# Performance work log

Measured on AMD Instinct MI355X. Metric: run time of the kernel, lower is better.

The kernel has to match this reference:

```python
import jax, jax.numpy as jnp
import numpy as np

EMBED = 1024
HEADS = 16
B, T = 2, 1024


def setup_inputs() -> dict:
    key = jax.random.key(0)
    k1, k2 = jax.random.split(key)
    x = jax.random.normal(k1, (B, T, EMBED), dtype=jnp.float32)
    # causal mask: True positions are masked to -inf (torch masked_fill semantics)
    mask = jnp.triu(jnp.ones((T, T), dtype=bool), k=1)
    weight = jax.random.normal(k2, (HEADS * EMBED, EMBED), dtype=jnp.float32)
    return {"x": x, "mask": mask, "weight": weight}


def reference(x, mask, weight):
    b, t, c = x.shape
    h = weight.shape[0] // c  # num_heads
    # split channels into heads: (b, h, t, head_dim)
    y = x.reshape(b, t, h, c // h).transpose(0, 2, 1, 3)
    # per-head scores (b, h, t, t)
    s = jnp.einsum('bhtk,bhsk->bhts', y, y)
    # mask BEFORE scaling, then scale by sqrt(num_heads) (not head_dim!)
    s = jnp.where(mask, -jnp.inf, s)
    p = jax.nn.softmax(s / jnp.sqrt(jnp.asarray(h, dtype=s.dtype)), axis=-1)
    # V is raw x broadcast across heads: (b, h, t, c)
    o = jnp.einsum('bhts,bsc->bhtc', p, x)
    # concat heads -> (b, t, h*c), final linear
    o = o.transpose(0, 2, 1, 3).reshape(b, t, h * c)
    return o @ weight
```

## Files before the change

### kernel.cpp

```cpp
#include <hip/hip_runtime.h>
#include <hip/hip_bf16.h>

#define B_ 2
#define T_ 1024
#define C_ 1024
#define H_ 16

typedef short bf16x8 __attribute__((ext_vector_type(8)));
typedef float f32x4 __attribute__((ext_vector_type(4)));

#define MFMA16(a, b, c) __builtin_amdgcn_mfma_f32_16x16x32_bf16(a, b, c, 0, 0, 0)

__device__ inline short f2bf(float x) {
    union { __hip_bfloat16 h; short s; } u;
    u.h = __float2bfloat16(x);
    return u.s;
}

__device__ inline void gl_lds16(const void* g, void* l) {
    __builtin_amdgcn_global_load_lds(
        (const __attribute__((address_space(1))) unsigned int*)g,
        (__attribute__((address_space(3))) unsigned int*)l, 16, 0, 0);
}

__global__ __launch_bounds__(256) void cvt_x(const float* __restrict__ x,
                                             short* __restrict__ xb) {
    int idx = (blockIdx.x * 256 + threadIdx.x) * 8;
    float4 a = *(const float4*)(x + idx);
    float4 b = *(const float4*)(x + idx + 4);
    bf16x8 v;
    v[0] = f2bf(a.x); v[1] = f2bf(a.y); v[2] = f2bf(a.z); v[3] = f2bf(a.w);
    v[4] = f2bf(b.x); v[5] = f2bf(b.y); v[6] = f2bf(b.z); v[7] = f2bf(b.w);
    *(bf16x8*)(xb + idx) = v;
}

__global__ __launch_bounds__(256) void cvt_w(const float* __restrict__ W,
                                             short* __restrict__ Wt) {
    __shared__ float T[64][65];
    const int bid = blockIdx.x;
    const int nb = bid & 15, cb = (bid >> 4) & 15, h = bid >> 8;
    const int t = threadIdx.x;
    const int c0 = cb * 64, n0 = nb * 64;
    const float* src = W + (size_t)(h * 1024 + c0) * 1024 + n0;
    {
        const int cl = t >> 4, nl = (t & 15) * 4;
#pragma unroll
        for (int r = 0; r < 4; ++r) {
            float4 v = *(const float4*)(src + (size_t)(cl + r * 16) * 1024 + nl);
            T[cl + r * 16][nl + 0] = v.x;
            T[cl + r * 16][nl + 1] = v.y;
            T[cl + r * 16][nl + 2] = v.z;
            T[cl + r * 16][nl + 3] = v.w;
        }
    }
    __syncthreads();
    {
        short* dst = Wt + (size_t)(h * 1024 + n0) * 1024 + c0;
        const int nl = t >> 3, cl8 = (t & 7) * 8;
#pragma unroll
        for (int r = 0; r < 2; ++r) {
            const int n = nl + r * 32;
            bf16x8 o;
#pragma unroll
            for (int j = 0; j < 8; ++j) o[j] = f2bf(T[cl8 + j][n]);
            *(bf16x8*)(dst + (size_t)n * 1024 + cl8) = o;
        }
    }
}

__global__ __launch_bounds__(512, 2) void attn_po(const short* __restrict__ xb,
                                                  const short* __restrict__ xbT,
                                                  short* __restrict__ O) {
    __shared__ short Pb[2][64][72];
    __shared__ float row_al[2][64];
    __shared__ float row_l[64];
    __shared__ int   flags[2][4];

    const int tid = threadIdx.x;
    const int bh = blockIdx.x & 31;
    const int rest = blockIdx.x >> 5;
    const int tb = (rest < 8) ? rest : 23 - rest;
    const int b = bh >> 4, h = bh & 15;
    const int lane = tid & 63, q = lane >> 4, l16 = lane & 15;
    const int w = tid >> 6;
    const int g = w & 3;
    const int nw = w * 128;
    const short* xbb = xb + ((size_t)b << 20);
    const short* vtb = xbT + ((size_t)b << 20);

    const int t0 = tb * 64;
    const int nch = tb + 1;

    f32x4 acc[4][8];
#pragma unroll
    for (int mt = 0; mt < 4; ++mt)
#pragma unroll
        for (int nt = 0; nt < 8; ++nt) acc[mt][nt] = (f32x4){0.f, 0.f, 0.f, 0.f};
    float m_r[4], l_r[4];
#pragma unroll
    for (int r = 0; r < 4; ++r) { m_r[r] = -3.0e38f; l_r[r] = 0.f; }

    bf16x8 qf[2];
    if (w < 4) {
#pragma unroll
        for (int ks = 0; ks < 2; ++ks)
            qf[ks] = *(const bf16x8*)(xbb + (size_t)(t0 + g * 16 + l16) * 1024 +
                                      h * 64 + ks * 32 + q * 8);
    }

    for (int ci = -1; ci < nch; ++ci) {
        __syncthreads();
        const int cc = ci + 1;
        if (w < 4 && cc < nch) {
            const int s0 = (cc == 0) ? t0 : (cc - 1) * 64;
            const int par = cc & 1;
            f32x4 sf[4];
#pragma unroll
            for (int st = 0; st < 4; ++st) sf[st] = (f32x4){0.f, 0.f, 0.f, 0.f};
#pragma unroll
            for (int st = 0; st < 4; ++st)
#pragma unroll
                for (int ks = 0; ks < 2; ++ks) {
                    bf16x8 kf = *(const bf16x8*)(xbb +
                        (size_t)(s0 + st * 16 + l16) * 1024 + h * 64 + ks * 32 + q * 8);
                    sf[st] = MFMA16(qf[ks], kf, sf[st]);
                }
            float mx[4] = {-3.0e38f, -3.0e38f, -3.0e38f, -3.0e38f};
#pragma unroll
            for (int st = 0; st < 4; ++st)
#pragma unroll
                for (int r = 0; r < 4; ++r) {
                    float v = sf[st][r] * 0.25f;
                    if (cc == 0 && (s0 + st * 16 + l16) > (t0 + g * 16 + q * 4 + r))
                        v = -3.0e38f;
                    sf[st][r] = v;
                    mx[r] = fmaxf(mx[r], v);
                }
#pragma unroll
            for (int r = 0; r < 4; ++r) {
                mx[r] = fmaxf(mx[r], __shfl_xor(mx[r], 1));
                mx[r] = fmaxf(mx[r], __shfl_xor(mx[r], 2));
                mx[r] = fmaxf(mx[r], __shfl_xor(mx[r], 4));
                mx[r] = fmaxf(mx[r], __shfl_xor(mx[r], 8));
            }
            float sum[4], al[4];
            int upd = 0;
#pragma unroll
            for (int r = 0; r < 4; ++r) {
                float m_new = fmaxf(m_r[r], mx[r]);
                al[r] = __expf(m_r[r] - m_new);
                upd |= (m_new > m_r[r]) ? 1 : 0;
                m_r[r] = m_new;
                sum[r] = 0.f;
            }
#pragma unroll
            for (int st = 0; st < 4; ++st)
#pragma unroll
                for (int r = 0; r < 4; ++r) {
                    float pv = __expf(sf[st][r] - m_r[r]);
                    sum[r] += pv;
                    Pb[par][g * 16 + q * 4 + r][st * 16 + l16] = f2bf(pv);
                }
#pragma unroll
            for (int r = 0; r < 4; ++r) {
                sum[r] += __shfl_xor(sum[r], 1);
                sum[r] += __shfl_xor(sum[r], 2);
                sum[r] += __shfl_xor(sum[r], 4);
                sum[r] += __shfl_xor(sum[r], 8);
                l_r[r] = l_r[r] * al[r] + sum[r];
            }
            if (l16 == 0) {
#pragma unroll
                for (int r = 0; r < 4; ++r) row_al[par][g * 16 + q * 4 + r] = al[r];
            }
            int any_upd = __any(upd);
            if (lane == 0) flags[par][g] = any_upd;
        }
        if (ci >= 0) {
            const int par = ci & 1;
            if (flags[par][0] | flags[par][1] | flags[par][2] | flags[par][3]) {
#pragma unroll
                for (int mt = 0; mt < 4; ++mt) {
                    float a0 = row_al[par][mt * 16 + q * 4 + 0];
                    float a1 = row_al[par][mt * 16 + q * 4 + 1];
                    float a2 = row_al[par][mt * 16 + q * 4 + 2];
                    float a3 = row_al[par][mt * 16 + q * 4 + 3];
#pragma unroll
                    for (int nt = 0; nt < 8; ++nt) {
                        acc[mt][nt][0] *= a0;
                        acc[mt][nt][1] *= a1;
                        acc[mt][nt][2] *= a2;
                        acc[mt][nt][3] *= a3;
                    }
                }
            }
            bf16x8 pf[4][2];
#pragma unroll
            for (int mt = 0; mt < 4; ++mt)
#pragma unroll
                for (int ks = 0; ks < 2; ++ks)
                    pf[mt][ks] = *(bf16x8*)&Pb[par][mt * 16 + l16][ks * 32 + q * 8];
            const int s0p = (ci == 0) ? t0 : (ci - 1) * 64;
#pragma unroll
            for (int nt = 0; nt < 8; ++nt)
#pragma unroll
                for (int ks = 0; ks < 2; ++ks) {
                    bf16x8 vf = *(const bf16x8*)(vtb +
                        (size_t)(nw + nt * 16 + l16) * 1024 + s0p + ks * 32 + q * 8);
#pragma unroll
                    for (int mt = 0; mt < 4; ++mt)
                        acc[mt][nt] = MFMA16(pf[mt][ks], vf, acc[mt][nt]);
                }
        }
    }

    if (w < 4 && l16 == 0) {
#pragma unroll
        for (int r = 0; r < 4; ++r) row_l[g * 16 + q * 4 + r] = l_r[r];
    }
    __syncthreads();
    short* ob = O + ((((size_t)(b * 1024 + t0) * 16) + h) << 10);
#pragma unroll
    for (int mt = 0; mt < 4; ++mt) {
        float i0 = 1.f / row_l[mt * 16 + q * 4 + 0];
        float i1 = 1.f / row_l[mt * 16 + q * 4 + 1];
        float i2 = 1.f / row_l[mt * 16 + q * 4 + 2];
        float i3 = 1.f / row_l[mt * 16 + q * 4 + 3];
#pragma unroll
        for (int nt = 0; nt < 8; ++nt) {
            size_t base = (size_t)(mt * 16 + q * 4) * 16384 + nw + nt * 16 + l16;
            ob[base]         = f2bf(acc[mt][nt][0] * i0);
            ob[base + 16384] = f2bf(acc[mt][nt][1] * i1);
            ob[base + 32768] = f2bf(acc[mt][nt][2] * i2);
            ob[base + 49152] = f2bf(acc[mt][nt][3] * i3);
        }
    }
}

__global__ __launch_bounds__(256, 4) void ogemm(const short* __restrict__ O,
                                                const short* __restrict__ Wt,
                                                float* __restrict__ out) {
    __shared__ short Al[8][128][8];
    __shared__ short Bl[8][128][8];

    const int orig = blockIdx.x;
    const int x = orig & 7, j = orig >> 3;
    const int kq  = x >> 1;
    const int m_t = (x & 1) * 8 + (j >> 3);
    const int n_t = j & 7;
    const int m0 = m_t * 128, n0 = n_t * 128;
    const int t = threadIdx.x;
    const int lane = t & 63, q = lane >> 4, l16 = lane & 15;
    const int wv = t >> 6;
    const int wm = (wv & 1) * 64, wn = (wv >> 1) * 64;

    const short* Ab = O + (size_t)m0 * 16384;
    const int srow = t & 127, skg = t >> 7;

    char* al_base = (char*)&Al[0][0][0] + (size_t)t * 16;
    char* bl_base = (char*)&Bl[0][0][0] + (size_t)t * 16;

    f32x4 acc[4][4];
#pragma unroll
    for (int i = 0; i < 4; ++i)
#pragma unroll
        for (int j2 = 0; j2 < 4; ++j2) acc[i][j2] = (f32x4){0.f, 0.f, 0.f, 0.f};

    const int kbase = kq * 4096;
    for (int kk = 0; kk < 4096; kk += 64) {
        const int k0 = kbase + kk;
        const int h = k0 >> 10, c0 = k0 & 1023;
        const short* Arow = Ab + (size_t)srow * 16384 + k0;
        const short* Brow = Wt + ((size_t)h << 20) + (size_t)(n0 + srow) * 1024 + c0;
        __syncthreads();
#pragma unroll
        for (int jj = 0; jj < 4; ++jj) {
            gl_lds16(Arow + (2 * jj + skg) * 8, al_base + jj * 4096);
            gl_lds16(Brow + (2 * jj + skg) * 8, bl_base + jj * 4096);
        }
        __syncthreads();
#pragma unroll
        for (int ks = 0; ks < 2; ++ks) {
            bf16x8 af[4], bfr[4];
#pragma unroll
            for (int i = 0; i < 4; ++i)
                af[i] = *(bf16x8*)&Al[q + 4 * ks][wm + i * 16 + l16][0];
#pragma unroll
            for (int j2 = 0; j2 < 4; ++j2)
                bfr[j2] = *(bf16x8*)&Bl[q + 4 * ks][wn + j2 * 16 + l16][0];
#pragma unroll
            for (int i = 0; i < 4; ++i)
#pragma unroll
                for (int j2 = 0; j2 < 4; ++j2)
                    acc[i][j2] = MFMA16(af[i], bfr[j2], acc[i][j2]);
        }
    }

#pragma unroll
    for (int i = 0; i < 4; ++i)
#pragma unroll
        for (int j2 = 0; j2 < 4; ++j2)
#pragma unroll
            for (int r = 0; r < 4; ++r) {
                int m = m0 + wm + i * 16 + q * 4 + r;
                int n = n0 + wn + j2 * 16 + l16;
                atomicAdd(out + (size_t)m * 1024 + n, acc[i][j2][r]);
            }
}

__global__ __launch_bounds__(256, 4) void zgemm_fast(const short* __restrict__ xb,
                                                     const short* __restrict__ Wt,
                                                     short* __restrict__ ZT) {
    __shared__ short Al[4][128][8];
    __shared__ short Bl[4][128][8];

    const int bid = blockIdx.x;
    const int n_t = bid & 7, h = (bid >> 3) & 15, s_t = bid >> 7;
    const int n0 = n_t * 128, s0g = s_t * 128;
    const int t = threadIdx.x;
    const int lane = t & 63, q = lane >> 4, l16 = lane & 15;
    const int wv = t >> 6;
    const int wm = (wv & 1) * 64, wn = (wv >> 1) * 64;

    const short* Ab = Wt + ((size_t)h * 1024 + n0) * 1024;
    const short* Bb = xb + (size_t)s0g * 1024;
    const int srow = t & 127, skg = t >> 7;

    char* al_base = (char*)&Al[0][0][0] + (size_t)t * 16;
    char* bl_base = (char*)&Bl[0][0][0] + (size_t)t * 16;

    f32x4 acc[4][4];
#pragma unroll
    for (int i = 0; i < 4; ++i)
#pragma unroll
        for (int j = 0; j < 4; ++j) acc[i][j] = (f32x4){0.f, 0.f, 0.f, 0.f};

    for (int k0 = 0; k0 < 1024; k0 += 32) {
        __syncthreads();
        gl_lds16(Ab + (size_t)srow * 1024 + k0 + skg * 8, al_base);
        gl_lds16(Ab + (size_t)srow * 1024 + k0 + (skg + 2) * 8, al_base + 4096);
        gl_lds16(Bb + (size_t)srow * 1024 + k0 + skg * 8, bl_base);
        gl_lds16(Bb + (size_t)srow * 1024 + k0 + (skg + 2) * 8, bl_base + 4096);
        __syncthreads();
        bf16x8 af[4], bfr[4];
#pragma unroll
        for (int i = 0; i < 4; ++i) af[i] = *(bf16x8*)&Al[q][wm + i * 16 + l16][0];
#pragma unroll
        for (int j = 0; j < 4; ++j) bfr[j] = *(bf16x8*)&Bl[q][wn + j * 16 + l16][0];
#pragma unroll
        for (int i = 0; i < 4; ++i)
#pragma unroll
            for (int j = 0; j < 4; ++j)
                acc[i][j] = MFMA16(af[i], bfr[j], acc[i][j]);
    }

    const int b = s0g >> 10, s_in0 = s0g & 1023;
    short* zb = ZT + ((size_t)(b * 16 + h) << 20);
#pragma unroll
    for (int i = 0; i < 4; ++i)
#pragma unroll
        for (int j = 0; j < 4; ++j)
#pragma unroll
            for (int r = 0; r < 4; ++r) {
                int n = n0 + wm + i * 16 + q * 4 + r;
                int s = s_in0 + wn + j * 16 + l16;
                zb[(size_t)n * 1024 + s] = f2bf(acc[i][j][r]);
            }
}

#define ZPAD 40

__global__ __launch_bounds__(256, 2) void zgemm_sm(const short* __restrict__ xb,
                                                   const float* __restrict__ W,
                                                   short* __restrict__ ZT) {
    __shared__ short Wts[128 * ZPAD];
    __shared__ short Xs[2][128 * ZPAD];

    const int tid = threadIdx.x;
    const int bs = blockIdx.x & 7;
    const int bn = (blockIdx.x >> 3) & 7;
    const int h  = blockIdx.x >> 6;
    const int s0 = bs * 128, n0 = bn * 128;
    const int lane = tid & 63, q = lane >> 4, l16 = lane & 15;
    const int w = tid >> 6, bw = w >> 1, sh = w & 1;

    f32x4 acc[8][4];
#pragma unroll
    for (int i = 0; i < 8; ++i)
#pragma unroll
        for (int j = 0; j < 4; ++j) acc[i][j] = (f32x4){0.f, 0.f, 0.f, 0.f};

    for (int k0 = 0; k0 < 1024; k0 += 32) {
        __syncthreads();
#pragma unroll
        for (int r = 0; r < 2; ++r) {
            const int c2 = ((tid >> 5) << 1) + (r << 4);
            const float* w0p = W + (size_t)(h * 1024 + k0 + c2) * 1024 + n0;
            const float* w1p = w0p + 1024;
#pragma unroll
            for (int i = 0; i < 4; ++i) {
                const int n = (tid & 31) + (i << 5);
                float wa = w0p[n], wb = w1p[n];
                unsigned u = (unsigned)(unsigned short)f2bf(wa) |
                             ((unsigned)(unsigned short)f2bf(wb) << 16);
                *(unsigned*)&Wts[n * ZPAD + c2] = u;
            }
        }
#pragma unroll
        for (int i = 0; i < 4; ++i) {
            const int id = tid + (i << 8);
            const int b2 = id >> 9, s = (id >> 2) & 127, cg = id & 3;
            bf16x8 v = *(const bf16x8*)(xb + (size_t)b2 * (T_ * C_) +
                                        (size_t)(s0 + s) * 1024 + k0 + cg * 8);
            *(bf16x8*)&Xs[b2][s * ZPAD + cg * 8] = v;
        }
        __syncthreads();

        bf16x8 af[8], bfr[4];
#pragma unroll
        for (int nt = 0; nt < 8; ++nt)
            af[nt] = *(bf16x8*)&Wts[(nt * 16 + l16) * ZPAD + q * 8];
#pragma unroll
        for (int st = 0; st < 4; ++st)
            bfr[st] = *(bf16x8*)&Xs[bw][(sh * 64 + st * 16 + l16) * ZPAD + q * 8];
#pragma unroll
        for (int nt = 0; nt < 8; ++nt)
#pragma unroll
            for (int st = 0; st < 4; ++st)
                acc[nt][st] = MFMA16(af[nt], bfr[st], acc[nt][st]);
    }

    short* zb = ZT + (size_t)(bw * 16 + h) * (1024 * 1024);
#pragma unroll
    for (int nt = 0; nt < 8; ++nt)
#pragma unroll
        for (int st = 0; st < 4; ++st)
#pragma unroll
            for (int r = 0; r < 4; ++r) {
                int n_abs = n0 + nt * 16 + q * 4 + r;
                int s_abs = s0 + sh * 64 + st * 16 + l16;
                zb[(size_t)n_abs * 1024 + s_abs] = f2bf(acc[nt][st][r]);
            }
}

__global__ __launch_bounds__(512, 2) void attn(const short* __restrict__ xb,
                                               const short* __restrict__ ZT,
                                               float* __restrict__ out) {
    __shared__ short Pb[2][64][72];
    __shared__ float row_al[2][64];
    __shared__ float row_l[64];
    __shared__ int   flags[2][4];

    const int tid = threadIdx.x;
    const int bh = blockIdx.x & 31, p = blockIdx.x >> 5;
    const int b = bh >> 4, h = bh & 15;
    const int lane = tid & 63, q = lane >> 4, l16 = lane & 15;
    const int w = tid >> 6;
    const int g = w & 3;
    const int nw = w * 128;
    const short* xbb = xb + ((size_t)b << 20);
    const short* ztb = ZT + ((size_t)(b * 16 + h) << 20);

    const int tiles[2] = { p, 15 - p };
    for (int ti = 0; ti < 2; ++ti) {
        const int tb = tiles[ti];
        const int t0 = tb * 64;
        const int nch = tb + 1;

        f32x4 acc[4][8];
#pragma unroll
        for (int mt = 0; mt < 4; ++mt)
#pragma unroll
            for (int nt = 0; nt < 8; ++nt) acc[mt][nt] = (f32x4){0.f, 0.f, 0.f, 0.f};
        float m_r[4], l_r[4];
#pragma unroll
        for (int r = 0; r < 4; ++r) { m_r[r] = -3.0e38f; l_r[r] = 0.f; }

        bf16x8 qf[2];
        if (w < 4) {
#pragma unroll
            for (int ks = 0; ks < 2; ++ks)
                qf[ks] = *(const bf16x8*)(xbb + (size_t)(t0 + g * 16 + l16) * 1024 +
                                          h * 64 + ks * 32 + q * 8);
        }

        for (int ci = -1; ci < nch; ++ci) {
            __syncthreads();
            const int cc = ci + 1;
            if (w < 4 && cc < nch) {
                const int s0 = (cc == 0) ? t0 : (cc - 1) * 64;
                const int par = cc & 1;
                f32x4 sf[4];
#pragma unroll
                for (int st = 0; st < 4; ++st) sf[st] = (f32x4){0.f, 0.f, 0.f, 0.f};
#pragma unroll
                for (int st = 0; st < 4; ++st)
#pragma unroll
                    for (int ks = 0; ks < 2; ++ks) {
                        bf16x8 kf = *(const bf16x8*)(xbb +
                            (size_t)(s0 + st * 16 + l16) * 1024 + h * 64 + ks * 32 + q * 8);
                        sf[st] = MFMA16(qf[ks], kf, sf[st]);
                    }
                float mx[4] = {-3.0e38f, -3.0e38f, -3.0e38f, -3.0e38f};
#pragma unroll
                for (int st = 0; st < 4; ++st)
#pragma unroll
                    for (int r = 0; r < 4; ++r) {
                        float v = sf[st][r] * 0.25f;
                        if (cc == 0 && (s0 + st * 16 + l16) > (t0 + g * 16 + q * 4 + r))
                            v = -3.0e38f;
                        sf[st][r] = v;
                        mx[r] = fmaxf(mx[r], v);
                    }
#pragma unroll
                for (int r = 0; r < 4; ++r) {
                    mx[r] = fmaxf(mx[r], __shfl_xor(mx[r], 1));
                    mx[r] = fmaxf(mx[r], __shfl_xor(mx[r], 2));
                    mx[r] = fmaxf(mx[r], __shfl_xor(mx[r], 4));
                    mx[r] = fmaxf(mx[r], __shfl_xor(mx[r], 8));
                }
                float sum[4], al[4];
                int upd = 0;
#pragma unroll
                for (int r = 0; r < 4; ++r) {
                    float m_new = fmaxf(m_r[r], mx[r]);
                    al[r] = __expf(m_r[r] - m_new);
                    upd |= (m_new > m_r[r]) ? 1 : 0;
                    m_r[r] = m_new;
                    sum[r] = 0.f;
                }
#pragma unroll
                for (int st = 0; st < 4; ++st)
#pragma unroll
                    for (int r = 0; r < 4; ++r) {
                        float pv = __expf(sf[st][r] - m_r[r]);
                        sum[r] += pv;
                        Pb[par][g * 16 + q * 4 + r][st * 16 + l16] = f2bf(pv);
                    }
#pragma unroll
                for (int r = 0; r < 4; ++r) {
                    sum[r] += __shfl_xor(sum[r], 1);
                    sum[r] += __shfl_xor(sum[r], 2);
                    sum[r] += __shfl_xor(sum[r], 4);
                    sum[r] += __shfl_xor(sum[r], 8);
                    l_r[r] = l_r[r] * al[r] + sum[r];
                }
                if (l16 == 0) {
#pragma unroll
                    for (int r = 0; r < 4; ++r) row_al[par][g * 16 + q * 4 + r] = al[r];
                }
                int any_upd = __any(upd);
                if (lane == 0) flags[par][g] = any_upd;
            }
            if (ci >= 0) {
                const int par = ci & 1;
                if (flags[par][0] | flags[par][1] | flags[par][2] | flags[par][3]) {
#pragma unroll
                    for (int mt = 0; mt < 4; ++mt) {
                        float a0 = row_al[par][mt * 16 + q * 4 + 0];
                        float a1 = row_al[par][mt * 16 + q * 4 + 1];
                        float a2 = row_al[par][mt * 16 + q * 4 + 2];
                        float a3 = row_al[par][mt * 16 + q * 4 + 3];
#pragma unroll
                        for (int nt = 0; nt < 8; ++nt) {
                            acc[mt][nt][0] *= a0;
                            acc[mt][nt][1] *= a1;
                            acc[mt][nt][2] *= a2;
                            acc[mt][nt][3] *= a3;
                        }
                    }
                }
                bf16x8 pf[4][2];
#pragma unroll
                for (int mt = 0; mt < 4; ++mt)
#pragma unroll
                    for (int ks = 0; ks < 2; ++ks)
                        pf[mt][ks] = *(bf16x8*)&Pb[par][mt * 16 + l16][ks * 32 + q * 8];
                const int s0p = (ci == 0) ? t0 : (ci - 1) * 64;
#pragma unroll
                for (int nt = 0; nt < 8; ++nt)
#pragma unroll
                    for (int ks = 0; ks < 2; ++ks) {
                        bf16x8 vf = *(const bf16x8*)(ztb +
                            (size_t)(nw + nt * 16 + l16) * 1024 + s0p + ks * 32 + q * 8);
#pragma unroll
                        for (int mt = 0; mt < 4; ++mt)
                            acc[mt][nt] = MFMA16(pf[mt][ks], vf, acc[mt][nt]);
                    }
            }
        }

        if (w < 4 && l16 == 0) {
#pragma unroll
            for (int r = 0; r < 4; ++r) row_l[g * 16 + q * 4 + r] = l_r[r];
        }
        __syncthreads();
#pragma unroll
        for (int mt = 0; mt < 4; ++mt) {
            float i0 = 1.f / row_l[mt * 16 + q * 4 + 0];
            float i1 = 1.f / row_l[mt * 16 + q * 4 + 1];
            float i2 = 1.f / row_l[mt * 16 + q * 4 + 2];
            float i3 = 1.f / row_l[mt * 16 + q * 4 + 3];
#pragma unroll
            for (int nt = 0; nt < 8; ++nt) {
                size_t base = (size_t)(b * 1024 + t0 + mt * 16 + q * 4) * 1024 +
                              nw + nt * 16 + l16;
                atomicAdd(out + base,            acc[mt][nt][0] * i0);
                atomicAdd(out + base + 1024,     acc[mt][nt][1] * i1);
                atomicAdd(out + base + 2048,     acc[mt][nt][2] * i2);
                atomicAdd(out + base + 3072,     acc[mt][nt][3] * i3);
            }
        }
        __syncthreads();
    }
}

extern "C" void kernel_launch(void* const* d_in, const int* in_sizes, int n_in,
                              void* d_out, int out_size, void* d_ws, size_t ws_size,
                              hipStream_t stream) {
    const float* x = (const float*)d_in[0];
    const float* W = (const float*)d_in[2];
    float* out = (float*)d_out;

    hipMemsetAsync(d_out, 0, (size_t)B_ * T_ * C_ * sizeof(float), stream);

    if (ws_size >= (size_t)104 * 1024 * 1024) {
        short* xb  = (short*)d_ws;
        short* xbT = xb + (size_t)2 * 1024 * 1024;
        short* Wt  = xb + (size_t)4 * 1024 * 1024;
        short* O   = xb + (size_t)20 * 1024 * 1024;

        cvt_x<<<(B_ * T_ * C_) / (256 * 8), 256, 0, stream>>>(x, xb);
        cvt_w<<<B_ * 16 * 16, 256, 0, stream>>>(x, xbT);
        cvt_w<<<16 * 16 * 16, 256, 0, stream>>>(W, Wt);
        attn_po<<<512, 512, 0, stream>>>(xb, xbT, O);
        ogemm<<<512, 256, 0, stream>>>(O, Wt, out);
    } else {
        short* xb = (short*)d_ws;
        short* ZT = (short*)d_ws + (size_t)B_ * T_ * C_;
        short* Wt = ZT + (size_t)B_ * H_ * 1024 * 1024;

        const bool big_ws = ws_size >= (size_t)100 * 1024 * 1024;
        cvt_x<<<(B_ * T_ * C_) / (256 * 8), 256, 0, stream>>>(x, xb);
        if (big_ws) {
            cvt_w<<<16 * 16 * 16, 256, 0, stream>>>(W, Wt);
            zgemm_fast<<<16 * 16 * 8, 256, 0, stream>>>(xb, Wt, ZT);
        } else {
            zgemm_sm<<<H_ * 8 * 8, 256, 0, stream>>>(xb, W, ZT);
        }
        attn<<<256, 512, 0, stream>>>(xb, ZT, out);
    }
}
```

Measured before the change: 363.2 us.

## Fuse input conversion kernels and widen ogemm N tile to 256

```diff
diff --git a/kernel.cpp b/kernel.cpp
--- a/kernel.cpp
+++ b/kernel.cpp
@@ -64,6 +64,58 @@
 #pragma unroll
             for (int j = 0; j < 8; ++j) o[j] = f2bf(T[cl8 + j][n]);
             *(bf16x8*)(dst + (size_t)n * 1024 + cl8) = o;
+        }
+    }
+}
+
+__global__ __launch_bounds__(256) void cvt_fused(const float* __restrict__ x,
+                                                 const float* __restrict__ W,
+                                                 short* __restrict__ xb,
+                                                 short* __restrict__ xbT,
+                                                 short* __restrict__ Wt) {
+    __shared__ float T[64][65];
+    const int bid0 = blockIdx.x;
+    const bool isX = bid0 < 512;
+    const int bid = isX ? bid0 : bid0 - 512;
+    const float* srcb = isX ? x : W;
+    short* dstb = isX ? xbT : Wt;
+    const int nb = bid & 15, cb = (bid >> 4) & 15, g = bid >> 8;
+    const int t = threadIdx.x;
+    const int c0 = cb * 64, n0 = nb * 64;
+    const float* src = srcb + (size_t)(g * 1024 + c0) * 1024 + n0;
+    {
+        const int cl = t >> 4, nl = (t & 15) * 4;
+#pragma unroll
+        for (int r = 0; r < 4; ++r) {
+            float4 v = *(const float4*)(src + (size_t)(cl + r * 16) * 1024 + nl);
+            T[cl + r * 16][nl + 0] = v.x;
+            T[cl + r * 16][nl + 1] = v.y;
+            T[cl + r * 16][nl + 2] = v.z;
+            T[cl + r * 16][nl + 3] = v.w;
+        }
+    }
+    __syncthreads();
+    {
+        short* dst = dstb + (size_t)(g * 1024 + n0) * 1024 + c0;
+        const int nl = t >> 3, cl8 = (t & 7) * 8;
+#pragma unroll
+        for (int r = 0; r < 2; ++r) {
+            const int n = nl + r * 32;
+            bf16x8 o;
+#pragma unroll
+            for (int j = 0; j < 8; ++j) o[j] = f2bf(T[cl8 + j][n]);
+            *(bf16x8*)(dst + (size_t)n * 1024 + cl8) = o;
+        }
+    }
+    if (isX) {
+        const int rl = t >> 3, c8 = (t & 7) * 8;
+#pragma unroll
+        for (int rr = 0; rr < 2; ++rr) {
+            const int row = rl + rr * 32;
+            bf16x8 o;
+#pragma unroll
+            for (int j = 0; j < 8; ++j) o[j] = f2bf(T[row][c8 + j]);
+            *(bf16x8*)(xb + (size_t)(g * 1024 + c0 + row) * 1024 + n0 + c8) = o;
         }
     }
 }
@@ -237,22 +289,22 @@
     }
 }
 
-__global__ __launch_bounds__(256, 4) void ogemm(const short* __restrict__ O,
+__global__ __launch_bounds__(256, 2) void ogemm(const short* __restrict__ O,
                                                 const short* __restrict__ Wt,
                                                 float* __restrict__ out) {
     __shared__ short Al[8][128][8];
-    __shared__ short Bl[8][128][8];
+    __shared__ short Bl[8][256][8];
 
     const int orig = blockIdx.x;
     const int x = orig & 7, j = orig >> 3;
-    const int kq  = x >> 1;
-    const int m_t = (x & 1) * 8 + (j >> 3);
-    const int n_t = j & 7;
-    const int m0 = m_t * 128, n0 = n_t * 128;
+    const int kq  = x;
+    const int m_t = j >> 2;
+    const int n_t = j & 3;
+    const int m0 = m_t * 128, n0 = n_t * 256;
     const int t = threadIdx.x;
     const int lane = t & 63, q = lane >> 4, l16 = lane & 15;
     const int wv = t >> 6;
-    const int wm = (wv & 1) * 64, wn = (wv >> 1) * 64;
+    const int wm = (wv & 1) * 64, wn = (wv >> 1) * 128;
 
     const short* Ab = O + (size_t)m0 * 16384;
     const int srow = t & 127, skg = t >> 7;
@@ -260,38 +312,39 @@
     char* al_base = (char*)&Al[0][0][0] + (size_t)t * 16;
     char* bl_base = (char*)&Bl[0][0][0] + (size_t)t * 16;
 
-    f32x4 acc[4][4];
+    f32x4 acc[4][8];
 #pragma unroll
     for (int i = 0; i < 4; ++i)
 #pragma unroll
-        for (int j2 = 0; j2 < 4; ++j2) acc[i][j2] = (f32x4){0.f, 0.f, 0.f, 0.f};
-
-    const int kbase = kq * 4096;
-    for (int kk = 0; kk < 4096; kk += 64) {
+        for (int j2 = 0; j2 < 8; ++j2) acc[i][j2] = (f32x4){0.f, 0.f, 0.f, 0.f};
+
+    const int kbase = kq * 2048;
+    for (int kk = 0; kk < 2048; kk += 64) {
         const int k0 = kbase + kk;
         const int h = k0 >> 10, c0 = k0 & 1023;
         const short* Arow = Ab + (size_t)srow * 16384 + k0;
-        const short* Brow = Wt + ((size_t)h << 20) + (size_t)(n0 + srow) * 1024 + c0;
-        __syncthreads();
-#pragma unroll
-        for (int jj = 0; jj < 4; ++jj) {
+        const short* Brow = Wt + ((size_t)h << 20) + (size_t)(n0 + t) * 1024 + c0;
+        __syncthreads();
+#pragma unroll
+        for (int jj = 0; jj < 4; ++jj)
             gl_lds16(Arow + (2 * jj + skg) * 8, al_base + jj * 4096);
-            gl_lds16(Brow + (2 * jj + skg) * 8, bl_base + jj * 4096);
-        }
+#pragma unroll
+        for (int kg = 0; kg < 8; ++kg)
+            gl_lds16(Brow + kg * 8, bl_base + kg * 4096);
         __syncthreads();
 #pragma unroll
         for (int ks = 0; ks < 2; ++ks) {
-            bf16x8 af[4], bfr[4];
+            bf16x8 af[4], bfr[8];
 #pragma unroll
             for (int i = 0; i < 4; ++i)
                 af[i] = *(bf16x8*)&Al[q + 4 * ks][wm + i * 16 + l16][0];
 #pragma unroll
-            for (int j2 = 0; j2 < 4; ++j2)
+            for (int j2 = 0; j2 < 8; ++j2)
                 bfr[j2] = *(bf16x8*)&Bl[q + 4 * ks][wn + j2 * 16 + l16][0];
 #pragma unroll
             for (int i = 0; i < 4; ++i)
 #pragma unroll
-                for (int j2 = 0; j2 < 4; ++j2)
+                for (int j2 = 0; j2 < 8; ++j2)
                     acc[i][j2] = MFMA16(af[i], bfr[j2], acc[i][j2]);
         }
     }
@@ -299,7 +352,7 @@
 #pragma unroll
     for (int i = 0; i < 4; ++i)
 #pragma unroll
-        for (int j2 = 0; j2 < 4; ++j2)
+        for (int j2 = 0; j2 < 8; ++j2)
 #pragma unroll
             for (int r = 0; r < 4; ++r) {
                 int m = m0 + wm + i * 16 + q * 4 + r;
@@ -630,9 +683,7 @@
         short* Wt  = xb + (size_t)4 * 1024 * 1024;
         short* O   = xb + (size_t)20 * 1024 * 1024;
 
-        cvt_x<<<(B_ * T_ * C_) / (256 * 8), 256, 0, stream>>>(x, xb);
-        cvt_w<<<B_ * 16 * 16, 256, 0, stream>>>(x, xbT);
-        cvt_w<<<16 * 16 * 16, 256, 0, stream>>>(W, Wt);
+        cvt_fused<<<512 + 4096, 256, 0, stream>>>(x, W, xb, xbT, Wt);
         attn_po<<<512, 512, 0, stream>>>(xb, xbT, O);
         ogemm<<<512, 256, 0, stream>>>(O, Wt, out);
     } else {
```

Result: no change. 369.5 us (+1.7%).
